# Performance work log

Hardware: AMD Instinct MI355X
Metric: run time of the kernel (lower is better)

Reference implementation:

```python
import jax, jax.numpy as jnp
import numpy as np

STRIDE = 4
H, W, A = 208, 336, 3
ANCHOR_SCALE = 8.0
ASPECTS = ((1.0, 1.0), (1.4, 0.7), (0.7, 1.4))  # (aspect_x, aspect_y)
PRE_NMS = 2000
POST_NMS = 1000
IOU_THR = 0.7
BBOX_CLIP = float(np.log(1000.0 / 16.0))


def make_anchors():
    # EfficientDet/SageMakerCV-style anchors at level 2, boxes as (y1, x1, y2, x2)
    base = ANCHOR_SCALE * STRIDE  # 32
    yc = (np.arange(H, dtype=np.float32) + 0.5) * STRIDE
    xc = (np.arange(W, dtype=np.float32) + 0.5) * STRIDE
    yy, xx = np.meshgrid(yc, xc, indexing='ij')  # [H, W]
    per_aspect = []
    for ax, ay in ASPECTS:
        hx, hy = base * ax / 2.0, base * ay / 2.0
        per_aspect.append(np.stack([yy - hy, xx - hx, yy + hy, xx + hx], axis=-1))
    return np.stack(per_aspect, axis=2).reshape(-1, 4).astype(np.float32)  # [H*W*A, 4]


def decode(deltas, anchors):
    # deltas: [B, N, 4] (dy, dx, dh, dw); anchors: [N, 4]; weights (1,1,1,1)
    ah = anchors[:, 2] - anchors[:, 0]
    aw = anchors[:, 3] - anchors[:, 1]
    acy = anchors[:, 0] + 0.5 * ah
    acx = anchors[:, 1] + 0.5 * aw
    dy, dx = deltas[..., 0], deltas[..., 1]
    dh = jnp.clip(deltas[..., 2], -BBOX_CLIP, BBOX_CLIP)
    dw = jnp.clip(deltas[..., 3], -BBOX_CLIP, BBOX_CLIP)
    cy = dy * ah + acy
    cx = dx * aw + acx
    h = jnp.exp(dh) * ah
    w = jnp.exp(dw) * aw
    return jnp.stack([cy - 0.5 * h, cx - 0.5 * w, cy + 0.5 * h, cx + 0.5 * w], axis=-1)


def _iou_one_to_many(box, boxes):
    y1 = jnp.maximum(box[0], boxes[:, 0])
    x1 = jnp.maximum(box[1], boxes[:, 1])
    y2 = jnp.minimum(box[2], boxes[:, 2])
    x2 = jnp.minimum(box[3], boxes[:, 3])
    inter = jnp.maximum(y2 - y1, 0.0) * jnp.maximum(x2 - x1, 0.0)
    a1 = (box[2] - box[0]) * (box[3] - box[1])
    a2 = (boxes[:, 2] - boxes[:, 0]) * (boxes[:, 3] - boxes[:, 1])
    return inter / (a1 + a2 - inter + 1e-8)


def nms_single(boxes, scores):
    # greedy NMS, fixed POST_NMS iterations (jit-friendly)
    def body(i, state):
        sc, kb, ks = state
        j = jnp.argmax(sc)
        b, s = boxes[j], sc[j]
        kb = kb.at[i].set(b)
        ks = ks.at[i].set(s)
        sup = _iou_one_to_many(b, boxes) > IOU_THR  # suppresses j itself (iou=1)
        sc = jnp.where(sup, -1.0, sc)
        return sc, kb, ks

    init = (scores,
            jnp.zeros((POST_NMS, 4), boxes.dtype),
            jnp.zeros((POST_NMS,), scores.dtype))
    _, kb, ks = jax.lax.fori_loop(0, POST_NMS, body, init)
    return kb, ks


def setup_inputs() -> dict:
    key = jax.random.key(0)
    k0, k1, k2 = jax.random.split(key, 3)
    feats = jax.random.normal(k0, (2, H, W, 256), dtype=jnp.float32)
    img_info = jnp.ones((2, 2), jnp.float32) * jnp.array([832.0, 1344.0], jnp.float32)
    w_cls = 0.01 * jax.random.normal(k1, (256, A * 1), dtype=jnp.float32)
    b_cls = jnp.zeros((A * 1,), jnp.float32)
    w_reg = 0.01 * jax.random.normal(k2, (256, A * 4), dtype=jnp.float32)
    b_reg = jnp.zeros((A * 4,), jnp.float32)
    return {"feats": feats, "img_info": img_info, "w_cls": w_cls, "b_cls": b_cls,
            "w_reg": w_reg, "b_reg": b_reg}


def reference(feats, img_info, w_cls, b_cls, w_reg, b_reg):
    B = feats.shape[0]
    # 1x1 convs == channel matmuls
    cls_scores = jnp.einsum('bhwc,co->bhwo', feats, w_cls) + b_cls  # [B,H,W,3]
    bbox_preds = jnp.einsum('bhwc,co->bhwo', feats, w_reg) + b_reg  # [B,H,W,12]

    scores = jax.nn.sigmoid(cls_scores).reshape(B, -1)       # [B, N]
    deltas = bbox_preds.reshape(B, -1, 4)                    # [B, N, 4]
    anchors = jnp.asarray(make_anchors())                    # [N, 4]
    boxes = decode(deltas, anchors)                          # [B, N, 4]

    # clip to image extents
    hmax = img_info[:, 0][:, None]
    wmax = img_info[:, 1][:, None]
    boxes = jnp.stack([
        jnp.clip(boxes[..., 0], 0.0, hmax),
        jnp.clip(boxes[..., 1], 0.0, wmax),
        jnp.clip(boxes[..., 2], 0.0, hmax),
        jnp.clip(boxes[..., 3], 0.0, wmax)], axis=-1)

    # per-image pre-NMS topk
    top_s, idx = jax.lax.top_k(scores, PRE_NMS)              # [B, PRE]
    top_b = jnp.take_along_axis(boxes, idx[..., None], axis=1)  # [B, PRE, 4]

    rois, roi_scores = jax.vmap(nms_single)(top_b, top_s)    # [B, POST, 4], [B, POST]
    return cls_scores, bbox_preds, rois, roi_scores
```

## Files before the change

kernel.cpp:

```cpp
#include <hip/hip_runtime.h>
#include <cstdint>
#include <cstddef>

#define HH 208
#define WW 336
#define NA 3
#define NPER 209664
#define NROWS 139776
#define RPI 69888
#define NB 2
#define PRE_K 2000
#define POST_K 1000
#define CAP 8192
#define MW 32
#define MROWS 2048
#define BBOX_CLIP_F 4.135166556742356f

#define WS_HIST   0
#define WS_HIST2  32768
#define WS_META   65536
#define WS_META24 65544
#define WS_CCNT   65552
#define WS_KEEPW  65568
#define WS_CAND   66080
#define WS_SBOX   197152
#define WS_SSC    261152
#define WS_MASK   277248
#define WS_ZERO_WORDS 16520

__device__ __forceinline__ float sigmoidf_ref(float x) {
  return __fdiv_rn(1.0f, __fadd_rn(1.0f, expf(-x)));
}
__device__ __forceinline__ unsigned int score_u(float logit) {
  float s = sigmoidf_ref(logit);
  return __float_as_uint(s) | 0x80000000u;
}

__device__ __forceinline__ unsigned long long bcast64(unsigned long long v, int l) {
  unsigned int lo = (unsigned int)__builtin_amdgcn_readlane((int)(unsigned int)v, l);
  unsigned int hi = (unsigned int)__builtin_amdgcn_readlane((int)(unsigned int)(v >> 32), l);
  return ((unsigned long long)hi << 32) | lo;
}

__device__ __forceinline__ float4 decode_box(const float* __restrict__ bbox,
                                             int b, unsigned int n,
                                             float hmax, float wmax) {
  unsigned int a = n % 3u;
  unsigned int pix = n / 3u;
  unsigned int y = pix / (unsigned int)WW;
  unsigned int x = pix % (unsigned int)WW;
  float yc = ((float)y + 0.5f) * 4.0f;
  float xc = ((float)x + 0.5f) * 4.0f;
  float hx = (a == 0) ? 16.0f : ((a == 1) ? 22.4f : 11.2f);
  float hy = (a == 0) ? 16.0f : ((a == 1) ? 11.2f : 22.4f);
  float ay1 = __fsub_rn(yc, hy), ax1 = __fsub_rn(xc, hx);
  float ay2 = __fadd_rn(yc, hy), ax2 = __fadd_rn(xc, hx);
  float ah = __fsub_rn(ay2, ay1), aw = __fsub_rn(ax2, ax1);
  float acy = __fadd_rn(ay1, __fmul_rn(0.5f, ah));
  float acx = __fadd_rn(ax1, __fmul_rn(0.5f, aw));
  const float* d = bbox + ((size_t)b * NPER + n) * 4u;
  float dy = d[0], dx = d[1];
  float dh = fminf(fmaxf(d[2], -BBOX_CLIP_F), BBOX_CLIP_F);
  float dw = fminf(fmaxf(d[3], -BBOX_CLIP_F), BBOX_CLIP_F);
  float cy = __fadd_rn(__fmul_rn(dy, ah), acy);
  float cx = __fadd_rn(__fmul_rn(dx, aw), acx);
  float hh = __fmul_rn(expf(dh), ah);
  float wwv = __fmul_rn(expf(dw), aw);
  float y1 = __fsub_rn(cy, __fmul_rn(0.5f, hh));
  float x1 = __fsub_rn(cx, __fmul_rn(0.5f, wwv));
  float y2 = __fadd_rn(cy, __fmul_rn(0.5f, hh));
  float x2 = __fadd_rn(cx, __fmul_rn(0.5f, wwv));
  y1 = fminf(fmaxf(y1, 0.0f), hmax);
  x1 = fminf(fmaxf(x1, 0.0f), wmax);
  y2 = fminf(fmaxf(y2, 0.0f), hmax);
  x2 = fminf(fmaxf(x2, 0.0f), wmax);
  return make_float4(y1, x1, y2, x2);
}

__device__ __forceinline__ float iou_ref(float4 bi, float4 bj) {
  float yA = fmaxf(bi.x, bj.x);
  float xA = fmaxf(bi.y, bj.y);
  float yB = fminf(bi.z, bj.z);
  float xB = fminf(bi.w, bj.w);
  float inter = __fmul_rn(fmaxf(__fsub_rn(yB, yA), 0.0f),
                          fmaxf(__fsub_rn(xB, xA), 0.0f));
  float a1 = __fmul_rn(__fsub_rn(bi.z, bi.x), __fsub_rn(bi.w, bi.y));
  float a2 = __fmul_rn(__fsub_rn(bj.z, bj.x), __fsub_rn(bj.w, bj.y));
  float den = __fadd_rn(__fsub_rn(__fadd_rn(a1, a2), inter), 1e-8f);
  return __fdiv_rn(inter, den);
}

__global__ void k_zero(unsigned int* __restrict__ p, int n) {
  int i = blockIdx.x * blockDim.x + threadIdx.x;
  if (i < n) p[i] = 0u;
}

__global__ __launch_bounds__(256, 3) void k_head(
    const float* __restrict__ feats, const float* __restrict__ w_cls,
    const float* __restrict__ b_cls, const float* __restrict__ w_reg,
    const float* __restrict__ b_reg, float* __restrict__ out_cls,
    float* __restrict__ out_bbox, unsigned int* __restrict__ hist) {
  const int b = blockIdx.y;
  const int lane = threadIdx.x & 63;
  const int wid = blockIdx.x * (blockDim.x >> 6) + (threadIdx.x >> 6);
  const int nw = gridDim.x * (blockDim.x >> 6);
  const int k0 = lane << 2;
  const int l15 = lane & 15;
  const int ol = ((l15 & 1) << 3) | ((l15 & 2) << 1) | ((l15 & 4) >> 1) |
                 ((l15 & 8) >> 3);

  __shared__ unsigned int h[4096];
  __shared__ float wt[16][256];
  for (int i = threadIdx.x; i < 4096; i += blockDim.x) {
    h[i] = 0u;
    const int o = i >> 8, c = i & 255;
    wt[o][c] = (o < 3) ? w_cls[c * 3 + o]
                       : (o < 15 ? w_reg[c * 12 + (o - 3)] : 0.0f);
  }
  __syncthreads();

  float4 w0  = *(const float4*)&wt[ol ^ 0][k0];
  float4 w1  = *(const float4*)&wt[ol ^ 1][k0];
  float4 w2  = *(const float4*)&wt[ol ^ 2][k0];
  float4 w3  = *(const float4*)&wt[ol ^ 3][k0];
  float4 w4  = *(const float4*)&wt[ol ^ 4][k0];
  float4 w5  = *(const float4*)&wt[ol ^ 5][k0];
  float4 w6  = *(const float4*)&wt[ol ^ 6][k0];
  float4 w7  = *(const float4*)&wt[ol ^ 7][k0];
  float4 w8  = *(const float4*)&wt[ol ^ 8][k0];
  float4 w9  = *(const float4*)&wt[ol ^ 9][k0];
  float4 w10 = *(const float4*)&wt[ol ^ 10][k0];
  float4 w11 = *(const float4*)&wt[ol ^ 11][k0];
  float4 w12 = *(const float4*)&wt[ol ^ 12][k0];
  float4 w13 = *(const float4*)&wt[ol ^ 13][k0];
  float4 w14 = *(const float4*)&wt[ol ^ 14][k0];
  float4 w15 = *(const float4*)&wt[ol ^ 15][k0];
  const float bias = (ol < 3) ? b_cls[ol] : (ol < 15 ? b_reg[ol - 3] : 0.0f);

  for (int rr = wid; rr < RPI; rr += 2 * nw) {
    const int rr1 = rr + nw;
    const int has1 = (rr1 < RPI);
    const int r0 = b * RPI + rr;
    const int r1 = b * RPI + (has1 ? rr1 : rr);
    const float4 f0 = *(const float4*)(feats + (size_t)r0 * 256 + k0);
    const float4 f1 = *(const float4*)(feats + (size_t)r1 * 256 + k0);
    float a0[16], a1[16];
#define STEPJ(J, W)                                                        \
    {                                                                      \
      a0[J] = f0.x * W.x; a0[J] += f0.y * W.y;                             \
      a0[J] += f0.z * W.z; a0[J] += f0.w * W.w;                            \
      a1[J] = f1.x * W.x; a1[J] += f1.y * W.y;                             \
      a1[J] += f1.z * W.z; a1[J] += f1.w * W.w;                            \
    }
    STEPJ(0, w0)   STEPJ(1, w1)   STEPJ(2, w2)   STEPJ(3, w3)
    STEPJ(4, w4)   STEPJ(5, w5)   STEPJ(6, w6)   STEPJ(7, w7)
    STEPJ(8, w8)   STEPJ(9, w9)   STEPJ(10, w10) STEPJ(11, w11)
    STEPJ(12, w12) STEPJ(13, w13) STEPJ(14, w14) STEPJ(15, w15)
#undef STEPJ
#pragma unroll
    for (int s = 0; s < 8; ++s) {
      a0[s] += __shfl_xor(a0[8 + s], 1, 64);
      a1[s] += __shfl_xor(a1[8 + s], 1, 64);
    }
#pragma unroll
    for (int s = 0; s < 4; ++s) {
      a0[s] += __shfl_xor(a0[4 + s], 2, 64);
      a1[s] += __shfl_xor(a1[4 + s], 2, 64);
    }
#pragma unroll
    for (int s = 0; s < 2; ++s) {
      a0[s] += __shfl_xor(a0[2 + s], 4, 64);
      a1[s] += __shfl_xor(a1[2 + s], 4, 64);
    }
    a0[0] += __shfl_xor(a0[1], 8, 64);
    a1[0] += __shfl_xor(a1[1], 8, 64);
    a0[0] += __shfl_xor(a0[0], 16, 64);
    a1[0] += __shfl_xor(a1[0], 16, 64);
    a0[0] += __shfl_xor(a0[0], 32, 64);
    a1[0] += __shfl_xor(a1[0], 32, 64);
    if (lane < 16 && ol < 15) {
      float v0 = a0[0] + bias;
      if (ol < 3) {
        out_cls[(size_t)r0 * 3 + ol] = v0;
        atomicAdd(&h[score_u(v0) >> 20], 1u);
      } else {
        out_bbox[(size_t)r0 * 12 + (ol - 3)] = v0;
      }
      if (has1) {
        float v1 = a1[0] + bias;
        if (ol < 3) {
          out_cls[(size_t)r1 * 3 + ol] = v1;
          atomicAdd(&h[score_u(v1) >> 20], 1u);
        } else {
          out_bbox[(size_t)r1 * 12 + (ol - 3)] = v1;
        }
      }
    }
  }
  __syncthreads();
  for (int i = threadIdx.x; i < 4096; i += blockDim.x)
    if (h[i]) atomicAdd(&hist[b * 4096 + i], h[i]);
}

__global__ __launch_bounds__(1024) void k_thresh(const unsigned int* __restrict__ hist,
                                                 unsigned int* __restrict__ meta_T) {
  const int b = blockIdx.x;
  const int t = threadIdx.x;
  __shared__ unsigned int sums[1024];
  unsigned int hb[4];
  unsigned int s = 0u;
#pragma unroll
  for (int q = 0; q < 4; ++q) {
    int bin = 4095 - (t * 4 + q);
    hb[q] = hist[b * 4096 + bin];
    s += hb[q];
  }
  sums[t] = s;
  __syncthreads();
  for (int off = 1; off < 1024; off <<= 1) {
    unsigned int v = (t >= off) ? sums[t - off] : 0u;
    __syncthreads();
    sums[t] += v;
    __syncthreads();
  }
  unsigned int excl = sums[t] - s;
  if (excl < PRE_K && excl + s >= PRE_K) {
    unsigned int c = excl;
#pragma unroll
    for (int q = 0; q < 4; ++q) {
      c += hb[q];
      if (c >= PRE_K) { meta_T[b] = (unsigned int)(4095 - (t * 4 + q)); break; }
    }
  }
}

__global__ __launch_bounds__(256) void k_hist2(const float* __restrict__ out_cls,
                                               const unsigned int* __restrict__ meta_T,
                                               unsigned int* __restrict__ hist2) {
  const int b = blockIdx.y;
  const unsigned int T = meta_T[b];
  __shared__ unsigned int h[4096];
  for (int i = threadIdx.x; i < 4096; i += blockDim.x) h[i] = 0u;
  __syncthreads();
  for (int i = blockIdx.x * blockDim.x + threadIdx.x; i < NPER;
       i += gridDim.x * blockDim.x) {
    unsigned int u = score_u(out_cls[(size_t)b * NPER + i]);
    if ((u >> 20) == T) atomicAdd(&h[(u >> 8) & 0xFFFu], 1u);
  }
  __syncthreads();
  for (int i = threadIdx.x; i < 4096; i += blockDim.x)
    if (h[i]) atomicAdd(&hist2[b * 4096 + i], h[i]);
}

__global__ __launch_bounds__(1024) void k_thresh2(const unsigned int* __restrict__ hist,
                                                  const unsigned int* __restrict__ hist2,
                                                  const unsigned int* __restrict__ meta_T,
                                                  unsigned int* __restrict__ meta_T24) {
  const int b = blockIdx.x;
  const int t = threadIdx.x;
  const unsigned int T = meta_T[b];
  __shared__ unsigned int sums[1024];
  __shared__ unsigned int c0s;
  unsigned int c0 = 0u;
  for (int i = t; i < 4096; i += 1024)
    if ((unsigned int)i > T) c0 += hist[b * 4096 + i];
  sums[t] = c0;
  __syncthreads();
  for (int off = 512; off > 0; off >>= 1) {
    if (t < off) sums[t] += sums[t + off];
    __syncthreads();
  }
  if (t == 0) c0s = sums[0];
  __syncthreads();
  const unsigned int C0 = c0s;
  __syncthreads();
  unsigned int hb[4];
  unsigned int s = 0u;
#pragma unroll
  for (int q = 0; q < 4; ++q) {
    int bin = 4095 - (t * 4 + q);
    hb[q] = hist2[b * 4096 + bin];
    s += hb[q];
  }
  sums[t] = s;
  __syncthreads();
  for (int off = 1; off < 1024; off <<= 1) {
    unsigned int v = (t >= off) ? sums[t - off] : 0u;
    __syncthreads();
    sums[t] += v;
    __syncthreads();
  }
  unsigned int excl = sums[t] - s;
  if (C0 + excl < PRE_K && C0 + excl + s >= PRE_K) {
    unsigned int c = C0 + excl;
#pragma unroll
    for (int q = 0; q < 4; ++q) {
      c += hb[q];
      if (c >= PRE_K) {
        meta_T24[b] = (T << 12) | (unsigned int)(4095 - (t * 4 + q));
        break;
      }
    }
  }
}

__global__ __launch_bounds__(256) void k_compact(const float* __restrict__ out_cls,
                                                 const unsigned int* __restrict__ meta_T24,
                                                 unsigned int* __restrict__ cand_count,
                                                 unsigned long long* __restrict__ cand) {
  const int b = blockIdx.y;
  const unsigned int T24 = meta_T24[b];
  for (int i = blockIdx.x * blockDim.x + threadIdx.x; i < NPER;
       i += gridDim.x * blockDim.x) {
    unsigned int u = score_u(out_cls[(size_t)b * NPER + i]);
    if ((u >> 8) >= T24) {
      unsigned int pos = atomicAdd(&cand_count[b], 1u);
      if (pos < CAP)
        cand[(size_t)b * CAP + pos] =
            ((unsigned long long)u << 32) | (unsigned int)(~(unsigned int)i);
    }
  }
}

__global__ __launch_bounds__(1024) void k_sort(const unsigned long long* __restrict__ cand,
                                               const unsigned int* __restrict__ cand_count,
                                               const float* __restrict__ out_bbox,
                                               const float* __restrict__ img_info,
                                               float* __restrict__ sboxes,
                                               float* __restrict__ sscores) {
  const int b = blockIdx.x;
  const int t = threadIdx.x;
  __shared__ unsigned long long keys[CAP];
  unsigned int cc = cand_count[b];
  if (cc > CAP) cc = CAP;
  int n = 2048;
  while ((unsigned int)n < cc) n <<= 1;
  for (int i = t; i < n; i += 1024)
    keys[i] = (i < (int)cc) ? cand[(size_t)b * CAP + i] : 0ull;
  __syncthreads();
  for (int k = 2; k <= n; k <<= 1) {
    for (int j = k >> 1; j > 0; j >>= 1) {
      for (int i = t; i < n; i += 1024) {
        int ixj = i ^ j;
        if (ixj > i) {
          unsigned long long a = keys[i], c = keys[ixj];
          bool up = ((i & k) == 0);
          bool sw = up ? (a < c) : (a > c);
          if (sw) { keys[i] = c; keys[ixj] = a; }
        }
      }
      __syncthreads();
    }
  }
  const float hmax = img_info[b * 2 + 0];
  const float wmax = img_info[b * 2 + 1];
  for (int i = t; i < PRE_K; i += 1024) {
    unsigned long long key = keys[i];
    unsigned int u = (unsigned int)(key >> 32);
    unsigned int idx = ~(unsigned int)(key & 0xFFFFFFFFull);
    float sc = __uint_as_float(u & 0x7FFFFFFFu);
    float4 bx = decode_box(out_bbox, b, idx, hmax, wmax);
    ((float4*)sboxes)[(size_t)b * PRE_K + i] = bx;
    sscores[(size_t)b * PRE_K + i] = sc;
  }
}

__global__ __launch_bounds__(64) void k_mask(const float* __restrict__ sboxes,
                                             unsigned long long* __restrict__ mask) {
  const int b = blockIdx.z;
  const int rb = blockIdx.x;
  const int cb = blockIdx.y;
  const int t = threadIdx.x;
  if (cb < rb) {
    int i = rb * 64 + t;
    if (i < PRE_K) mask[((size_t)b * MROWS + i) * MW + cb] = 0ull;
    return;
  }
  __shared__ float4 cbox[64];
  const int col0 = cb * 64;
  {
    int c = col0 + t;
    cbox[t] = (c < PRE_K) ? ((const float4*)sboxes)[(size_t)b * PRE_K + c]
                          : make_float4(0.f, 0.f, 0.f, 0.f);
  }
  __syncthreads();
  const int i = rb * 64 + t;
  if (i >= PRE_K) return;
  float4 bi = ((const float4*)sboxes)[(size_t)b * PRE_K + i];
  unsigned long long bits = 0ull;
#pragma unroll 8
  for (int j = 0; j < 64; ++j) {
    int c = col0 + j;
    if (c > i && c < PRE_K) {
      if (iou_ref(bi, cbox[j]) > 0.7f) bits |= (1ull << j);
    }
  }
  mask[((size_t)b * MROWS + i) * MW + cb] = bits;
}

#define MLOAD(BUF, G)                                                     \
  {                                                                       \
    _Pragma("unroll") for (int _k = 0; _k < 32; ++_k) {                   \
      int _row = (G) * 64 + 2 * _k + psel;                                \
      (BUF)[_k] = (_row < PRE_K) ? M[(size_t)(G) * 2048 + 64 * _k + lane] \
                                 : 0ull;                                  \
    }                                                                     \
  }
#define DLOAD(DST, G)                                                     \
  {                                                                       \
    int _row = (G) * 64 + lane;                                           \
    (DST) = ((G) < 32 && _row < PRE_K) ? M[(size_t)_row * MW + (G)] : 0ull; \
  }
#define GSTEP(G, MCUR, MNEXT, DCUR, DNEXT)                                \
  do {                                                                    \
    MLOAD(MNEXT, (G) + 1);                                                \
    DLOAD(DNEXT, (G) + 1);                                                \
    unsigned long long w = bcast64(remv, (G)) | bcast64(remv, (G) + 32);  \
    unsigned long long alive = ~w;                                        \
    if ((G) == 31) alive &= (1ull << (PRE_K - 31 * 64)) - 1ull;           \
    unsigned long long kept = 0ull;                                       \
    while (alive) {                                                       \
      int j = __builtin_ctzll(alive);                                     \
      unsigned long long bit = 1ull << j;                                 \
      kept |= bit;                                                        \
      unsigned long long dj = bcast64((DCUR), j);                         \
      alive &= ~(dj | bit);                                               \
    }                                                                     \
    int pc = __popcll(kept);                                              \
    if (nk + pc >= POST_K) {                                              \
      int need = POST_K - nk;                                             \
      unsigned long long k2 = kept;                                       \
      for (int _t = 0; _t < need; ++_t) k2 &= k2 - 1;                     \
      kept ^= k2;                \
      if (lane == 0) keepw[b * 32 + (G)] = kept;                          \
      stop = 1;                                                           \
    } else {                                                              \
      nk += pc;                                                           \
      if (lane == 0) keepw[b * 32 + (G)] = kept;                          \
      unsigned long long keptv = kept >> psel;                            \
      _Pragma("unroll") for (int _q = 0; _q < 32; ++_q) {                 \
        unsigned long long sel = 0ull - ((keptv >> (2 * _q)) & 1ull);     \
        remv |= (MCUR)[_q] & sel;                                         \
      }                                                                   \
    }                                                                     \
  } while (0)

__global__ __launch_bounds__(64, 1) void k_scan(
    const unsigned long long* __restrict__ mask,
    unsigned long long* __restrict__ keepw) {
  const int b = blockIdx.x;
  const int lane = threadIdx.x;
  const int psel = lane >> 5;
  const unsigned long long* M = mask + (size_t)b * MROWS * MW;

  unsigned long long mbA[32], mbB[32], dA, dB;
  unsigned long long remv = 0ull;
  int nk = 0, stop = 0;

  MLOAD(mbA, 0);
  DLOAD(dA, 0);
  for (int g = 0; g < 32; g += 2) {
    GSTEP(g, mbA, mbB, dA, dB);
    if (stop) break;
    GSTEP(g + 1, mbB, mbA, dB, dA);
    if (stop) break;
  }
}

__global__ __launch_bounds__(64) void k_write(const float* __restrict__ sboxes,
                                              const float* __restrict__ sscores,
                                              const unsigned long long* __restrict__ keepw,
                                              float* __restrict__ rois,
                                              float* __restrict__ rsc) {
  const int b = blockIdx.x;
  const int lane = threadIdx.x;
  unsigned long long w = (lane < 32) ? keepw[b * 32 + lane] : 0ull;
  int pc = __popcll(w);
  int pref = pc;
#pragma unroll
  for (int off = 1; off < 64; off <<= 1) {
    int v = __shfl_up(pref, off, 64);
    if (lane >= off) pref += v;
  }
  const int excl = pref - pc;
  const int Ktot = __shfl(pref, 63, 64);
  int rank = excl;
  unsigned long long ww = w;
  while (ww) {
    int j = __builtin_ctzll(ww);
    ww &= ww - 1;
    int row = lane * 64 + j;
    ((float4*)rois)[(size_t)b * POST_K + rank] =
        ((const float4*)sboxes)[(size_t)b * PRE_K + row];
    rsc[(size_t)b * POST_K + rank] = sscores[(size_t)b * PRE_K + row];
    ++rank;
  }
  float4 pad = ((const float4*)sboxes)[(size_t)b * PRE_K + 0];
  for (int i = Ktot + lane; i < POST_K; i += 64) {
    ((float4*)rois)[(size_t)b * POST_K + i] = pad;
    rsc[(size_t)b * POST_K + i] = -1.0f;
  }
}

extern "C" void kernel_launch(void* const* d_in, const int* in_sizes, int n_in,
                              void* d_out, int out_size, void* d_ws, size_t ws_size,
                              hipStream_t stream) {
  const float* feats    = (const float*)d_in[0];
  const float* img_info = (const float*)d_in[1];
  const float* w_cls    = (const float*)d_in[2];
  const float* b_cls    = (const float*)d_in[3];
  const float* w_reg    = (const float*)d_in[4];
  const float* b_reg    = (const float*)d_in[5];

  float* out = (float*)d_out;
  float* out_cls  = out;
  float* out_bbox = out + 419328;
  float* out_rois = out + 2096640;
  float* out_rsc  = out + 2104640;

  char* ws = (char*)d_ws;
  unsigned int* hist        = (unsigned int*)(ws + WS_HIST);
  unsigned int* hist2       = (unsigned int*)(ws + WS_HIST2);
  unsigned int* meta_T      = (unsigned int*)(ws + WS_META);
  unsigned int* meta_T24    = (unsigned int*)(ws + WS_META24);
  unsigned int* cand_count  = (unsigned int*)(ws + WS_CCNT);
  unsigned long long* keepw = (unsigned long long*)(ws + WS_KEEPW);
  unsigned long long* cand  = (unsigned long long*)(ws + WS_CAND);
  float* sboxes             = (float*)(ws + WS_SBOX);
  float* sscores            = (float*)(ws + WS_SSC);
  unsigned long long* mask  = (unsigned long long*)(ws + WS_MASK);

  k_zero<<<(WS_ZERO_WORDS + 255) / 256, 256, 0, stream>>>((unsigned int*)ws, WS_ZERO_WORDS);
  k_head<<<dim3(512, NB), 256, 0, stream>>>(feats, w_cls, b_cls, w_reg, b_reg,
                                            out_cls, out_bbox, hist);
  k_thresh<<<NB, 1024, 0, stream>>>(hist, meta_T);
  k_hist2<<<dim3(128, NB), 256, 0, stream>>>(out_cls, meta_T, hist2);
  k_thresh2<<<NB, 1024, 0, stream>>>(hist, hist2, meta_T, meta_T24);
  k_compact<<<dim3(128, NB), 256, 0, stream>>>(out_cls, meta_T24, cand_count, cand);
  k_sort<<<NB, 1024, 0, stream>>>(cand, cand_count, out_bbox, img_info, sboxes, sscores);
  k_mask<<<dim3(32, 32, NB), 64, 0, stream>>>(sboxes, mask);
  k_scan<<<NB, 64, 0, stream>>>(mask, keepw);
  k_write<<<NB, 64, 0, stream>>>(sboxes, sscores, keepw, out_rois, out_rsc);
}
```

Before: 394.3 us.

## Prefetch next feature rows in head loop and fuse NMS write into scan

The head kernel's row loop is software-pipelined: the feature float4 loads for the next pair of rows are issued before computing the current pair, hiding global load latency. Separately, the keep-mask words are kept in registers per lane inside k_scan and the output-writing stage is folded into the same kernel, which removes the k_write launch and the keepw workspace round trip (and shrinks the zeroed workspace). The prefetch raises register pressure in the head kernel.

Measured after the change: 395.7 us. No clear change (+0.4%).

```diff
diff --git a/kernel.cpp b/kernel.cpp
--- a/kernel.cpp
+++ b/kernel.cpp
@@ -26,7 +26,7 @@
 #define WS_SBOX   197152
 #define WS_SSC    261152
 #define WS_MASK   277248
-#define WS_ZERO_WORDS 16520
+#define WS_ZERO_WORDS 16392
 
 __device__ __forceinline__ float sigmoidf_ref(float x) {
   return __fdiv_rn(1.0f, __fadd_rn(1.0f, expf(-x)));
@@ -137,13 +137,23 @@
   float4 w15 = *(const float4*)&wt[ol ^ 15][k0];
   const float bias = (ol < 3) ? b_cls[ol] : (ol < 15 ? b_reg[ol - 3] : 0.0f);
 
-  for (int rr = wid; rr < RPI; rr += 2 * nw) {
-    const int rr1 = rr + nw;
-    const int has1 = (rr1 < RPI);
+  const float* fb = feats + (size_t)b * RPI * 256 + k0;
+
+  int rr = wid;
+  int cr0 = rr;
+  int cr1 = (rr + nw < RPI) ? rr + nw : rr;
+  float4 f0 = *(const float4*)(fb + (size_t)cr0 * 256);
+  float4 f1 = *(const float4*)(fb + (size_t)cr1 * 256);
+
+  while (rr < RPI) {
+    const int has1 = (rr + nw < RPI);
     const int r0 = b * RPI + rr;
-    const int r1 = b * RPI + (has1 ? rr1 : rr);
-    const float4 f0 = *(const float4*)(feats + (size_t)r0 * 256 + k0);
-    const float4 f1 = *(const float4*)(feats + (size_t)r1 * 256 + k0);
+    const int r1 = b * RPI + (has1 ? rr + nw : rr);
+    const int nx = rr + 2 * nw;
+    const int n0 = (nx < RPI) ? nx : cr0;
+    const int n1 = (nx + nw < RPI) ? nx + nw : n0;
+    const float4 g0 = *(const float4*)(fb + (size_t)n0 * 256);
+    const float4 g1 = *(const float4*)(fb + (size_t)n1 * 256);
     float a0[16], a1[16];
 #define STEPJ(J, W)                                                        \
     {                                                                      \
@@ -196,6 +206,11 @@
         }
       }
     }
+    rr = nx;
+    cr0 = n0;
+    cr1 = n1;
+    f0 = g0;
+    f1 = g1;
   }
   __syncthreads();
   for (int i = threadIdx.x; i < 4096; i += blockDim.x)
@@ -432,11 +447,11 @@
       unsigned long long k2 = kept;                                       \
       for (int _t = 0; _t < need; ++_t) k2 &= k2 - 1;                     \
       kept ^= k2;                \
-      if (lane == 0) keepw[b * 32 + (G)] = kept;                          \
+      if (lane == (G)) mykeep = kept;                                     \
       stop = 1;                                                           \
     } else {                                                              \
       nk += pc;                                                           \
-      if (lane == 0) keepw[b * 32 + (G)] = kept;                          \
+      if (lane == (G)) mykeep = kept;                                     \
       unsigned long long keptv = kept >> psel;                            \
       _Pragma("unroll") for (int _q = 0; _q < 32; ++_q) {                 \
         unsigned long long sel = 0ull - ((keptv >> (2 * _q)) & 1ull);     \
@@ -447,7 +462,10 @@
 
 __global__ __launch_bounds__(64, 1) void k_scan(
     const unsigned long long* __restrict__ mask,
-    unsigned long long* __restrict__ keepw) {
+    const float* __restrict__ sboxes,
+    const float* __restrict__ sscores,
+    float* __restrict__ rois,
+    float* __restrict__ rsc) {
   const int b = blockIdx.x;
   const int lane = threadIdx.x;
   const int psel = lane >> 5;
@@ -455,6 +473,7 @@
 
   unsigned long long mbA[32], mbB[32], dA, dB;
   unsigned long long remv = 0ull;
+  unsigned long long mykeep = 0ull;
   int nk = 0, stop = 0;
 
   MLOAD(mbA, 0);
@@ -465,17 +484,8 @@
     GSTEP(g + 1, mbB, mbA, dB, dA);
     if (stop) break;
   }
-}
-
-__global__ __launch_bounds__(64) void k_write(const float* __restrict__ sboxes,
-                                              const float* __restrict__ sscores,
-                                              const unsigned long long* __restrict__ keepw,
-                                              float* __restrict__ rois,
-                                              float* __restrict__ rsc) {
-  const int b = blockIdx.x;
-  const int lane = threadIdx.x;
-  unsigned long long w = (lane < 32) ? keepw[b * 32 + lane] : 0ull;
-  int pc = __popcll(w);
+
+  int pc = __popcll(mykeep);
   int pref = pc;
 #pragma unroll
   for (int off = 1; off < 64; off <<= 1) {
@@ -485,7 +495,7 @@
   const int excl = pref - pc;
   const int Ktot = __shfl(pref, 63, 64);
   int rank = excl;
-  unsigned long long ww = w;
+  unsigned long long ww = mykeep;
   while (ww) {
     int j = __builtin_ctzll(ww);
     ww &= ww - 1;
@@ -524,7 +534,6 @@
   unsigned int* meta_T      = (unsigned int*)(ws + WS_META);
   unsigned int* meta_T24    = (unsigned int*)(ws + WS_META24);
   unsigned int* cand_count  = (unsigned int*)(ws + WS_CCNT);
-  unsigned long long* keepw = (unsigned long long*)(ws + WS_KEEPW);
   unsigned long long* cand  = (unsigned long long*)(ws + WS_CAND);
   float* sboxes             = (float*)(ws + WS_SBOX);
   float* sscores            = (float*)(ws + WS_SSC);
@@ -539,6 +548,5 @@
   k_compact<<<dim3(128, NB), 256, 0, stream>>>(out_cls, meta_T24, cand_count, cand);
   k_sort<<<NB, 1024, 0, stream>>>(cand, cand_count, out_bbox, img_info, sboxes, sscores);
   k_mask<<<dim3(32, 32, NB), 64, 0, stream>>>(sboxes, mask);
-  k_scan<<<NB, 64, 0, stream>>>(mask, keepw);
-  k_write<<<NB, 64, 0, stream>>>(sboxes, sscores, keepw, out_rois, out_rsc);
-}
+  k_scan<<<NB, 64, 0, stream>>>(mask, sboxes, sscores, out_rois, out_rsc);
+}
```

## Fuse pipeline stages with last-block-done atomics to cut kernel launches

Applied to the files above, without the earlier changes.

Folds the threshold, threshold2, sort, scan and write stages into the tails of the preceding kernels. A global atomic counter elects the last finishing block to run the dependent serial step, which takes the launch count from ten to five and removes the inter-kernel gaps. The compaction kernel now runs 32 blocks of 1024 threads instead of 128 of 256, and the keep words stay in registers instead of going through global memory. The cost is that the serial tail work now runs inside a single late block, with threadfence overhead and a reliance on memory-ordering correctness.

Result: slower. 576.8 us (+46.3%).

```diff
diff --git a/kernel.cpp b/kernel.cpp
--- a/kernel.cpp
+++ b/kernel.cpp
@@ -19,9 +19,6 @@
 #define WS_HIST   0
 #define WS_HIST2  32768
 #define WS_META   65536
-#define WS_META24 65544
-#define WS_CCNT   65552
-#define WS_KEEPW  65568
 #define WS_CAND   66080
 #define WS_SBOX   197152
 #define WS_SSC    261152
@@ -40,6 +37,43 @@
   unsigned int lo = (unsigned int)__builtin_amdgcn_readlane((int)(unsigned int)v, l);
   unsigned int hi = (unsigned int)__builtin_amdgcn_readlane((int)(unsigned int)(v >> 32), l);
   return ((unsigned long long)hi << 32) | lo;
+}
+
+__device__ __forceinline__ void suffix_select(const unsigned int* __restrict__ H,
+                                              unsigned int C0in, unsigned int need,
+                                              unsigned int base,
+                                              unsigned int* __restrict__ csum,
+                                              unsigned int* __restrict__ outBin,
+                                              unsigned int* __restrict__ outC0) {
+  const int t = threadIdx.x;
+  unsigned int hb[16];
+  unsigned int s = 0u;
+#pragma unroll
+  for (int q = 0; q < 16; ++q) {
+    hb[q] = H[4095 - (t * 16 + q)];
+    s += hb[q];
+  }
+  csum[t] = s;
+  __syncthreads();
+  for (int off = 1; off < 256; off <<= 1) {
+    unsigned int v = (t >= off) ? csum[t - off] : 0u;
+    __syncthreads();
+    csum[t] += v;
+    __syncthreads();
+  }
+  unsigned int excl = C0in + (csum[t] - s);
+  if (excl < need && excl + s >= need) {
+    unsigned int c = excl;
+#pragma unroll
+    for (int q = 0; q < 16; ++q) {
+      c += hb[q];
+      if (c >= need) {
+        *outBin = base | (unsigned int)(4095 - (t * 16 + q));
+        if (outC0) *outC0 = c - hb[q];
+        break;
+      }
+    }
+  }
 }
 
 __device__ __forceinline__ float4 decode_box(const float* __restrict__ bbox,
@@ -99,7 +133,8 @@
     const float* __restrict__ feats, const float* __restrict__ w_cls,
     const float* __restrict__ b_cls, const float* __restrict__ w_reg,
     const float* __restrict__ b_reg, float* __restrict__ out_cls,
-    float* __restrict__ out_bbox, unsigned int* __restrict__ hist) {
+    float* __restrict__ out_bbox, unsigned int* __restrict__ hist,
+    unsigned int* __restrict__ meta) {
   const int b = blockIdx.y;
   const int lane = threadIdx.x & 63;
   const int wid = blockIdx.x * (blockDim.x >> 6) + (threadIdx.x >> 6);
@@ -111,6 +146,7 @@
 
   __shared__ unsigned int h[4096];
   __shared__ float wt[16][256];
+  __shared__ int lastf;
   for (int i = threadIdx.x; i < 4096; i += blockDim.x) {
     h[i] = 0u;
     const int o = i >> 8, c = i & 255;
@@ -200,46 +236,25 @@
   __syncthreads();
   for (int i = threadIdx.x; i < 4096; i += blockDim.x)
     if (h[i]) atomicAdd(&hist[b * 4096 + i], h[i]);
-}
-
-__global__ __launch_bounds__(1024) void k_thresh(const unsigned int* __restrict__ hist,
-                                                 unsigned int* __restrict__ meta_T) {
-  const int b = blockIdx.x;
-  const int t = threadIdx.x;
-  __shared__ unsigned int sums[1024];
-  unsigned int hb[4];
-  unsigned int s = 0u;
-#pragma unroll
-  for (int q = 0; q < 4; ++q) {
-    int bin = 4095 - (t * 4 + q);
-    hb[q] = hist[b * 4096 + bin];
-    s += hb[q];
-  }
-  sums[t] = s;
-  __syncthreads();
-  for (int off = 1; off < 1024; off <<= 1) {
-    unsigned int v = (t >= off) ? sums[t - off] : 0u;
-    __syncthreads();
-    sums[t] += v;
-    __syncthreads();
-  }
-  unsigned int excl = sums[t] - s;
-  if (excl < PRE_K && excl + s >= PRE_K) {
-    unsigned int c = excl;
-#pragma unroll
-    for (int q = 0; q < 4; ++q) {
-      c += hb[q];
-      if (c >= PRE_K) { meta_T[b] = (unsigned int)(4095 - (t * 4 + q)); break; }
-    }
-  }
-}
-
-__global__ __launch_bounds__(256) void k_hist2(const float* __restrict__ out_cls,
-                                               const unsigned int* __restrict__ meta_T,
-                                               unsigned int* __restrict__ hist2) {
+
+  __threadfence();
+  __syncthreads();
+  if (threadIdx.x == 0)
+    lastf = (atomicAdd(&meta[8 + b], 1u) == gridDim.x - 1);
+  __syncthreads();
+  if (lastf) {
+    __threadfence();
+    suffix_select(hist + b * 4096, 0u, PRE_K, 0u, h, &meta[b], &meta[2 + b]);
+  }
+}
+
+__global__ __launch_bounds__(256) void k_h2t(const float* __restrict__ out_cls,
+                                             unsigned int* __restrict__ hist2,
+                                             unsigned int* __restrict__ meta) {
   const int b = blockIdx.y;
-  const unsigned int T = meta_T[b];
+  const unsigned int T = meta[b];
   __shared__ unsigned int h[4096];
+  __shared__ int lastf;
   for (int i = threadIdx.x; i < 4096; i += blockDim.x) h[i] = 0u;
   __syncthreads();
   for (int i = blockIdx.x * blockDim.x + threadIdx.x; i < NPER;
@@ -250,88 +265,50 @@
   __syncthreads();
   for (int i = threadIdx.x; i < 4096; i += blockDim.x)
     if (h[i]) atomicAdd(&hist2[b * 4096 + i], h[i]);
-}
-
-__global__ __launch_bounds__(1024) void k_thresh2(const unsigned int* __restrict__ hist,
-                                                  const unsigned int* __restrict__ hist2,
-                                                  const unsigned int* __restrict__ meta_T,
-                                                  unsigned int* __restrict__ meta_T24) {
-  const int b = blockIdx.x;
+
+  __threadfence();
+  __syncthreads();
+  if (threadIdx.x == 0)
+    lastf = (atomicAdd(&meta[10 + b], 1u) == gridDim.x - 1);
+  __syncthreads();
+  if (lastf) {
+    __threadfence();
+    suffix_select(hist2 + b * 4096, meta[2 + b], PRE_K, T << 12, h,
+                  &meta[4 + b], nullptr);
+  }
+}
+
+__global__ __launch_bounds__(1024) void k_cs(const float* __restrict__ out_cls,
+                                             unsigned int* __restrict__ meta,
+                                             unsigned long long* __restrict__ cand,
+                                             const float* __restrict__ out_bbox,
+                                             const float* __restrict__ img_info,
+                                             float* __restrict__ sboxes,
+                                             float* __restrict__ sscores) {
+  const int b = blockIdx.y;
   const int t = threadIdx.x;
-  const unsigned int T = meta_T[b];
-  __shared__ unsigned int sums[1024];
-  __shared__ unsigned int c0s;
-  unsigned int c0 = 0u;
-  for (int i = t; i < 4096; i += 1024)
-    if ((unsigned int)i > T) c0 += hist[b * 4096 + i];
-  sums[t] = c0;
-  __syncthreads();
-  for (int off = 512; off > 0; off >>= 1) {
-    if (t < off) sums[t] += sums[t + off];
-    __syncthreads();
-  }
-  if (t == 0) c0s = sums[0];
-  __syncthreads();
-  const unsigned int C0 = c0s;
-  __syncthreads();
-  unsigned int hb[4];
-  unsigned int s = 0u;
-#pragma unroll
-  for (int q = 0; q < 4; ++q) {
-    int bin = 4095 - (t * 4 + q);
-    hb[q] = hist2[b * 4096 + bin];
-    s += hb[q];
-  }
-  sums[t] = s;
-  __syncthreads();
-  for (int off = 1; off < 1024; off <<= 1) {
-    unsigned int v = (t >= off) ? sums[t - off] : 0u;
-    __syncthreads();
-    sums[t] += v;
-    __syncthreads();
-  }
-  unsigned int excl = sums[t] - s;
-  if (C0 + excl < PRE_K && C0 + excl + s >= PRE_K) {
-    unsigned int c = C0 + excl;
-#pragma unroll
-    for (int q = 0; q < 4; ++q) {
-      c += hb[q];
-      if (c >= PRE_K) {
-        meta_T24[b] = (T << 12) | (unsigned int)(4095 - (t * 4 + q));
-        break;
-      }
-    }
-  }
-}
-
-__global__ __launch_bounds__(256) void k_compact(const float* __restrict__ out_cls,
-                                                 const unsigned int* __restrict__ meta_T24,
-                                                 unsigned int* __restrict__ cand_count,
-                                                 unsigned long long* __restrict__ cand) {
-  const int b = blockIdx.y;
-  const unsigned int T24 = meta_T24[b];
-  for (int i = blockIdx.x * blockDim.x + threadIdx.x; i < NPER;
+  const unsigned int T24 = meta[4 + b];
+  __shared__ unsigned long long keys[CAP];
+  __shared__ int lastf;
+  for (int i = blockIdx.x * blockDim.x + t; i < NPER;
        i += gridDim.x * blockDim.x) {
     unsigned int u = score_u(out_cls[(size_t)b * NPER + i]);
     if ((u >> 8) >= T24) {
-      unsigned int pos = atomicAdd(&cand_count[b], 1u);
+      unsigned int pos = atomicAdd(&meta[6 + b], 1u);
       if (pos < CAP)
         cand[(size_t)b * CAP + pos] =
             ((unsigned long long)u << 32) | (unsigned int)(~(unsigned int)i);
     }
   }
-}
-
-__global__ __launch_bounds__(1024) void k_sort(const unsigned long long* __restrict__ cand,
-                                               const unsigned int* __restrict__ cand_count,
-                                               const float* __restrict__ out_bbox,
-                                               const float* __restrict__ img_info,
-                                               float* __restrict__ sboxes,
-                                               float* __restrict__ sscores) {
-  const int b = blockIdx.x;
-  const int t = threadIdx.x;
-  __shared__ unsigned long long keys[CAP];
-  unsigned int cc = cand_count[b];
+
+  __threadfence();
+  __syncthreads();
+  if (t == 0) lastf = (atomicAdd(&meta[12 + b], 1u) == gridDim.x - 1);
+  __syncthreads();
+  if (!lastf) return;
+  __threadfence();
+
+  unsigned int cc = meta[6 + b];
   if (cc > CAP) cc = CAP;
   int n = 2048;
   while ((unsigned int)n < cc) n <<= 1;
@@ -363,39 +340,6 @@
     ((float4*)sboxes)[(size_t)b * PRE_K + i] = bx;
     sscores[(size_t)b * PRE_K + i] = sc;
   }
-}
-
-__global__ __launch_bounds__(64) void k_mask(const float* __restrict__ sboxes,
-                                             unsigned long long* __restrict__ mask) {
-  const int b = blockIdx.z;
-  const int rb = blockIdx.x;
-  const int cb = blockIdx.y;
-  const int t = threadIdx.x;
-  if (cb < rb) {
-    int i = rb * 64 + t;
-    if (i < PRE_K) mask[((size_t)b * MROWS + i) * MW + cb] = 0ull;
-    return;
-  }
-  __shared__ float4 cbox[64];
-  const int col0 = cb * 64;
-  {
-    int c = col0 + t;
-    cbox[t] = (c < PRE_K) ? ((const float4*)sboxes)[(size_t)b * PRE_K + c]
-                          : make_float4(0.f, 0.f, 0.f, 0.f);
-  }
-  __syncthreads();
-  const int i = rb * 64 + t;
-  if (i >= PRE_K) return;
-  float4 bi = ((const float4*)sboxes)[(size_t)b * PRE_K + i];
-  unsigned long long bits = 0ull;
-#pragma unroll 8
-  for (int j = 0; j < 64; ++j) {
-    int c = col0 + j;
-    if (c > i && c < PRE_K) {
-      if (iou_ref(bi, cbox[j]) > 0.7f) bits |= (1ull << j);
-    }
-  }
-  mask[((size_t)b * MROWS + i) * MW + cb] = bits;
 }
 
 #define MLOAD(BUF, G)                                                     \
@@ -432,11 +376,11 @@
       unsigned long long k2 = kept;                                       \
       for (int _t = 0; _t < need; ++_t) k2 &= k2 - 1;                     \
       kept ^= k2;                \
-      if (lane == 0) keepw[b * 32 + (G)] = kept;                          \
+      if (lane == (G)) mykeep = kept;                                     \
       stop = 1;                                                           \
     } else {                                                              \
       nk += pc;                                                           \
-      if (lane == 0) keepw[b * 32 + (G)] = kept;                          \
+      if (lane == (G)) mykeep = kept;                                     \
       unsigned long long keptv = kept >> psel;                            \
       _Pragma("unroll") for (int _q = 0; _q < 32; ++_q) {                 \
         unsigned long long sel = 0ull - ((keptv >> (2 * _q)) & 1ull);     \
@@ -445,16 +389,60 @@
     }                                                                     \
   } while (0)
 
-__global__ __launch_bounds__(64, 1) void k_scan(
-    const unsigned long long* __restrict__ mask,
-    unsigned long long* __restrict__ keepw) {
-  const int b = blockIdx.x;
-  const int lane = threadIdx.x;
+__global__ __launch_bounds__(64) void k_ms(const float* __restrict__ sboxes,
+                                           const float* __restrict__ sscores,
+                                           unsigned long long* __restrict__ mask,
+                                           unsigned int* __restrict__ meta,
+                                           float* __restrict__ rois,
+                                           float* __restrict__ rsc) {
+  const int b = blockIdx.z;
+  const int rb = blockIdx.x;
+  const int cb = blockIdx.y;
+  const int t = threadIdx.x;
+  __shared__ float4 cbox[64];
+  __shared__ int lastf;
+
+  if (cb < rb) {
+    int i = rb * 64 + t;
+    if (i < PRE_K) mask[((size_t)b * MROWS + i) * MW + cb] = 0ull;
+  } else {
+    const int col0 = cb * 64;
+    {
+      int c = col0 + t;
+      cbox[t] = (c < PRE_K) ? ((const float4*)sboxes)[(size_t)b * PRE_K + c]
+                            : make_float4(0.f, 0.f, 0.f, 0.f);
+    }
+    __syncthreads();
+    const int i = rb * 64 + t;
+    if (i < PRE_K) {
+      float4 bi = ((const float4*)sboxes)[(size_t)b * PRE_K + i];
+      unsigned long long bits = 0ull;
+#pragma unroll 8
+      for (int j = 0; j < 64; ++j) {
+        int c = col0 + j;
+        if (c > i && c < PRE_K) {
+          if (iou_ref(bi, cbox[j]) > 0.7f) bits |= (1ull << j);
+        }
+      }
+      mask[((size_t)b * MROWS + i) * MW + cb] = bits;
+    }
+  }
+
+  __threadfence();
+  __syncthreads();
+  if (t == 0)
+    lastf = (atomicAdd(&meta[14 + b], 1u) == gridDim.x * gridDim.y - 1);
+  __syncthreads();
+  if (!lastf) return;
+  __threadfence();
+
+  const int lane = t;
   const int psel = lane >> 5;
   const unsigned long long* M = mask + (size_t)b * MROWS * MW;
 
   unsigned long long mbA[32], mbB[32], dA, dB;
   unsigned long long remv = 0ull;
+  unsigned long long mykeep = 0ull;
   int nk = 0, stop = 0;
 
   MLOAD(mbA, 0);
@@ -465,17 +453,8 @@
     GSTEP(g + 1, mbB, mbA, dB, dA);
     if (stop) break;
   }
-}
-
-__global__ __launch_bounds__(64) void k_write(const float* __restrict__ sboxes,
-                                              const float* __restrict__ sscores,
-                                              const unsigned long long* __restrict__ keepw,
-                                              float* __restrict__ rois,
-                                              float* __restrict__ rsc) {
-  const int b = blockIdx.x;
-  const int lane = threadIdx.x;
-  unsigned long long w = (lane < 32) ? keepw[b * 32 + lane] : 0ull;
-  int pc = __popcll(w);
+
+  int pc = __popcll(mykeep);
   int pref = pc;
 #pragma unroll
   for (int off = 1; off < 64; off <<= 1) {
@@ -485,7 +464,7 @@
   const int excl = pref - pc;
   const int Ktot = __shfl(pref, 63, 64);
   int rank = excl;
-  unsigned long long ww = w;
+  unsigned long long ww = mykeep;
   while (ww) {
     int j = __builtin_ctzll(ww);
     ww &= ww - 1;
@@ -521,10 +500,7 @@
   char* ws = (char*)d_ws;
   unsigned int* hist        = (unsigned int*)(ws + WS_HIST);
   unsigned int* hist2       = (unsigned int*)(ws + WS_HIST2);
-  unsigned int* meta_T      = (unsigned int*)(ws + WS_META);
-  unsigned int* meta_T24    = (unsigned int*)(ws + WS_META24);
-  unsigned int* cand_count  = (unsigned int*)(ws + WS_CCNT);
-  unsigned long long* keepw = (unsigned long long*)(ws + WS_KEEPW);
+  unsigned int* meta        = (unsigned int*)(ws + WS_META);
   unsigned long long* cand  = (unsigned long long*)(ws + WS_CAND);
   float* sboxes             = (float*)(ws + WS_SBOX);
   float* sscores            = (float*)(ws + WS_SSC);
@@ -532,13 +508,10 @@
 
   k_zero<<<(WS_ZERO_WORDS + 255) / 256, 256, 0, stream>>>((unsigned int*)ws, WS_ZERO_WORDS);
   k_head<<<dim3(512, NB), 256, 0, stream>>>(feats, w_cls, b_cls, w_reg, b_reg,
-                                            out_cls, out_bbox, hist);
-  k_thresh<<<NB, 1024, 0, stream>>>(hist, meta_T);
-  k_hist2<<<dim3(128, NB), 256, 0, stream>>>(out_cls, meta_T, hist2);
-  k_thresh2<<<NB, 1024, 0, stream>>>(hist, hist2, meta_T, meta_T24);
-  k_compact<<<dim3(128, NB), 256, 0, stream>>>(out_cls, meta_T24, cand_count, cand);
-  k_sort<<<NB, 1024, 0, stream>>>(cand, cand_count, out_bbox, img_info, sboxes, sscores);
-  k_mask<<<dim3(32, 32, NB), 64, 0, stream>>>(sboxes, mask);
-  k_scan<<<NB, 64, 0, stream>>>(mask, keepw);
-  k_write<<<NB, 64, 0, stream>>>(sboxes, sscores, keepw, out_rois, out_rsc);
-}
+                                            out_cls, out_bbox, hist, meta);
+  k_h2t<<<dim3(128, NB), 256, 0, stream>>>(out_cls, hist2, meta);
+  k_cs<<<dim3(32, NB), 1024, 0, stream>>>(out_cls, meta, cand, out_bbox,
+                                          img_info, sboxes, sscores);
+  k_ms<<<dim3(32, 32, NB), 64, 0, stream>>>(sboxes, sscores, mask, meta,
+                                            out_rois, out_rsc);
+}
```
